# Optimization experiments

Measured on AMD Instinct MI355X. Metric: run time of the kernel, lower is better.

The kernel has to match this reference:

```python
import math
import jax, jax.numpy as jnp
import numpy as np

ALPHA = 1.000001   # sparsity_alpha
N_ITER = 50        # entmax_bisect default bisection iterations
EPS = 1e-40        # training-mode epsilon inside log

B, T = 2, 1024
V, C, H, L = 50304, 768, 12, 4
DINT = 64
INT_BIAS0 = 5.0


def _entmax_impl(X):
    # alpha-entmax over last dim via bisection (entmax package algorithm)
    am1 = ALPHA - 1.0
    d = X.shape[-1]
    Xs = X * am1
    max_val = jnp.max(Xs, axis=-1, keepdims=True)
    tau_lo = max_val - 1.0
    tau_hi = max_val - (1.0 / d) ** am1
    f_lo = jnp.sum(jnp.clip(Xs - tau_lo, 0.0) ** (1.0 / am1), axis=-1, keepdims=True) - 1.0
    dm = tau_hi - tau_lo
    p_m = jnp.zeros_like(Xs)
    for _ in range(N_ITER):
        dm = dm * 0.5
        tau_m = tau_lo + dm
        p_m = jnp.clip(Xs - tau_m, 0.0) ** (1.0 / am1)
        f_m = jnp.sum(p_m, axis=-1, keepdims=True) - 1.0
        tau_lo = jnp.where(f_m * f_lo >= 0, tau_m, tau_lo)
    return p_m / jnp.sum(p_m, axis=-1, keepdims=True)


@jax.custom_vjp
def entmax_bisect(X):
    return _entmax_impl(X)


def _entmax_fwd(X):
    Y = _entmax_impl(X)
    return Y, Y


def _entmax_bwd(Y, dY):
    # exact entmax jacobian-vector product (as in the torch entmax package)
    gppr = jnp.where(Y > 0, Y ** (2.0 - ALPHA), 0.0)
    dX = dY * gppr
    q = jnp.sum(dX, axis=-1, keepdims=True) / jnp.sum(gppr, axis=-1, keepdims=True)
    return (dX - q * gppr,)


entmax_bisect.defvjp(_entmax_fwd, _entmax_bwd)


def layer_norm(x, w, b):
    mu = jnp.mean(x, axis=-1, keepdims=True)
    var = jnp.mean((x - mu) ** 2, axis=-1, keepdims=True)
    return (x - mu) / jnp.sqrt(var + 1e-5) * w + b


def new_gelu(x):
    return 0.5 * x * (1.0 + jnp.tanh(math.sqrt(2.0 / math.pi) * (x + 0.044715 * x ** 3)))


def gpt_forward(wte, wpe, ln1_w, ln1_b, attn_w, attn_b, qint_w, kint_w, int_bias,
                proj_w, proj_b, ln2_w, ln2_b, fc_w, fc_b, fc2_w, fc2_b,
                lnf_w, lnf_b, idx):
    Bc, Tc = idx.shape
    hd = C // H
    x = wte[idx] + wpe[:Tc][None]                       # [B,T,C]
    i = jnp.arange(Tc)
    strict_lower = i[:, None] > i[None, :]              # bias_int = tril(diag=-1)
    causal = i[:, None] >= i[None, :]                   # bias = tril
    prev_mask = None
    for l in range(L):
        h = layer_norm(x, ln1_w[l], ln1_b[l])
        qkv = h @ attn_w[l].T + attn_b[l]
        q, k, v = jnp.split(qkv, 3, axis=-1)
        q = q.reshape(Bc, Tc, H, hd).transpose(0, 2, 1, 3)
        k = k.reshape(Bc, Tc, H, hd).transpose(0, 2, 1, 3)
        v = v.reshape(Bc, Tc, H, hd).transpose(0, 2, 1, 3)
        # integer-gate scores
        q_int = h @ qint_w[l].T                         # [B,T,DINT]
        k_int = h @ kint_w[l].T
        raw = jnp.einsum('bqd,bkd->bqk', q_int, k_int) / math.sqrt(DINT) + int_bias[l]
        raw2 = jnp.stack([raw, jnp.zeros_like(raw)], axis=-1)[:, None]  # [B,1,T,T,2]
        p_int = entmax_bisect(raw2.astype(jnp.float32))[..., 0]        # [B,1,T,T]
        p_int = jnp.where(strict_lower[None, None], p_int, 1.0)         # fill j>=i with 1
        cumprobs = jnp.cumprod(p_int, axis=-2)                          # cumprod over queries
        attn_mask = jnp.log(cumprobs + EPS)
        if prev_mask is not None:                        # propagate_in_depth=True
            attn_mask = attn_mask + prev_mask
        attn_mask = jnp.where(causal[None, None], attn_mask, -jnp.inf)
        scores = jnp.einsum('bhqd,bhkd->bhqk', q, k) / math.sqrt(hd) + attn_mask
        att = jax.nn.softmax(scores, axis=-1)
        y = jnp.einsum('bhqk,bhkd->bhqd', att, v)
        y = y.transpose(0, 2, 1, 3).reshape(Bc, Tc, C)
        y = y @ proj_w[l].T + proj_b[l]
        x = x + y
        h2 = layer_norm(x, ln2_w[l], ln2_b[l])
        x = x + (new_gelu(h2 @ fc_w[l].T + fc_b[l]) @ fc2_w[l].T + fc2_b[l])
        prev_mask = attn_mask
    x = layer_norm(x, lnf_w, lnf_b)
    return x @ wte.T                                     # weight-tied lm_head


def setup_inputs() -> dict:
    key = jax.random.key(0)
    ks = jax.random.split(key, 9)
    f32 = jnp.float32
    return {
        'wte': jax.random.normal(ks[0], (V, C), f32) * 0.02,
        'wpe': jax.random.normal(ks[1], (1024, C), f32) * 0.02,
        'ln1_w': jnp.ones((L, C), f32),
        'ln1_b': jnp.zeros((L, C), f32),
        'attn_w': jax.random.normal(ks[2], (L, 3 * C, C), f32) * 0.02,
        'attn_b': jnp.zeros((L, 3 * C), f32),
        'qint_w': jax.random.normal(ks[3], (L, DINT, C), f32) / math.sqrt(C),
        'kint_w': jax.random.normal(ks[4], (L, DINT, C), f32) / math.sqrt(C),
        'int_bias': jnp.full((L,), INT_BIAS0, f32),
        'proj_w': jax.random.normal(ks[5], (L, C, C), f32) * (0.02 / math.sqrt(2 * L)),
        'proj_b': jnp.zeros((L, C), f32),
        'ln2_w': jnp.ones((L, C), f32),
        'ln2_b': jnp.zeros((L, C), f32),
        'fc_w': jax.random.normal(ks[6], (L, 4 * C, C), f32) * 0.02,
        'fc_b': jnp.zeros((L, 4 * C), f32),
        'fc2_w': jax.random.normal(ks[7], (L, C, 4 * C), f32) * (0.02 / math.sqrt(2 * L)),
        'fc2_b': jnp.zeros((L, C), f32),
        'lnf_w': jnp.ones((C,), f32),
        'lnf_b': jnp.zeros((C,), f32),
        'idx': jax.random.randint(ks[8], (B, T), 0, V, dtype=jnp.int32),
    }


def reference(wte, wpe, ln1_w, ln1_b, attn_w, attn_b, qint_w, kint_w, int_bias,
              proj_w, proj_b, ln2_w, ln2_b, fc_w, fc_b, fc2_w, fc2_b,
              lnf_w, lnf_b, idx):
    return gpt_forward(wte, wpe, ln1_w, ln1_b, attn_w, attn_b, qint_w, kint_w,
                       int_bias, proj_w, proj_b, ln2_w, ln2_b, fc_w, fc_b,
                       fc2_w, fc2_b, lnf_w, lnf_b, idx)
```

## Files before the change

### kernel.cpp

```cpp
#include <hip/hip_runtime.h>


using f32x4  = __attribute__((ext_vector_type(4))) float;
using bf16x8 = __attribute__((ext_vector_type(8))) __bf16;
typedef unsigned short u16;
typedef unsigned int   u32;

#define B_  2
#define T_  1024
#define C_  768
#define H_  12
#define HD_ 64
#define L_  4
#define V_  50304

__device__ __forceinline__ u16 f2bf(float f){
  u32 u = __float_as_uint(f);
  u += 0x7fffu + ((u >> 16) & 1u);
  return (u16)(u >> 16);
}

__device__ __forceinline__ void gld_lds16(const u16* gsrc, u16* ldsbase){
  __builtin_amdgcn_global_load_lds(
      (const __attribute__((address_space(1))) void*)gsrc,
      (__attribute__((address_space(3))) void*)ldsbase, 16, 0, 0);
}

__global__ __launch_bounds__(256) void f2bf_vec(const float4* __restrict__ src,
                                                ushort4* __restrict__ dst){
  long i = (long)blockIdx.x * 256 + threadIdx.x;
  float4 v = src[i];
  ushort4 o;
  o.x = f2bf(v.x); o.y = f2bf(v.y); o.z = f2bf(v.z); o.w = f2bf(v.w);
  dst[i] = o;
}

__global__ __launch_bounds__(256) void build_wint(const float* __restrict__ qint_w,
                                                  const float* __restrict__ kint_w,
                                                  u16* __restrict__ wint){
  long i = (long)blockIdx.x * 256 + threadIdx.x;
  int c  = (int)(i % 768);
  long r = i / 768;
  int rr = (int)(r & 127);
  int l  = (int)(r >> 7);
  const float* src = (rr < 64) ? qint_w : kint_w;
  wint[i] = f2bf(src[((long)l * 64 + (rr & 63)) * 768 + c]);
}

__global__ __launch_bounds__(256) void embed_kernel(const float* __restrict__ wte,
                                                    const float* __restrict__ wpe,
                                                    const int* __restrict__ idx,
                                                    float* __restrict__ x){
  int row = blockIdx.x;
  int t   = row & (T_ - 1);
  int id  = idx[row];
  const float* ws = wte + (long)id * C_;
  const float* ps = wpe + (long)t  * C_;
  float* xr = x + (long)row * C_;
  for (int c = threadIdx.x; c < C_; c += 256) xr[c] = ws[c] + ps[c];
}

__global__ __launch_bounds__(256) void layernorm_bf16(const float* __restrict__ x,
                                                      const float* __restrict__ w,
                                                      const float* __restrict__ bsh,
                                                      u16* __restrict__ out){
  int row = blockIdx.x;
  const float* xr = x + (long)row * C_;
  int tid = threadIdx.x;
  float v[3], s = 0.f, ss = 0.f;
  #pragma unroll
  for (int k = 0; k < 3; ++k){
    float t = xr[tid + k * 256];
    v[k] = t; s += t; ss += t * t;
  }
  #pragma unroll
  for (int off = 1; off < 64; off <<= 1){
    s  += __shfl_xor(s,  off, 64);
    ss += __shfl_xor(ss, off, 64);
  }
  __shared__ float red[8];
  int wid = tid >> 6, lane = tid & 63;
  if (lane == 0){ red[wid] = s; red[4 + wid] = ss; }
  __syncthreads();
  s  = red[0] + red[1] + red[2] + red[3];
  ss = red[4] + red[5] + red[6] + red[7];
  float mu   = s * (1.f / C_);
  float var  = ss * (1.f / C_) - mu * mu;
  float rstd = rsqrtf(var + 1e-5f);
  u16* outr = out + (long)row * C_;
  #pragma unroll
  for (int k = 0; k < 3; ++k){
    int c = tid + k * 256;
    outr[c] = f2bf((v[k] - mu) * rstd * w[c] + bsh[c]);
  }
}

template<int BM, int BN, int WM, int WN, bool GELU>
__global__ __launch_bounds__(256) void gemm_nt(
    const u16* __restrict__ A, const u16* __restrict__ B, float* __restrict__ C,
    const float* __restrict__ bias, const float* __restrict__ addsrc,
    int K, int lda, int ldb, int ldc,
    long batchA, long batchB, long batchC, float alpha)
{
  constexpr int BK = 32;
  __shared__ __align__(16) u16 As[BM * BK];
  __shared__ __align__(16) u16 Bs[BN * BK];
  const int z = blockIdx.z;
  A += (long)z * batchA;
  B += (long)z * batchB;
  float* Cz = C + (long)z * batchC;
  const float* addz = addsrc ? addsrc + (long)z * batchC : nullptr;

  const int gx = gridDim.x, gy = gridDim.y;
  const int nwg = gx * gy;
  int bid = blockIdx.y * gx + blockIdx.x;
  {
    int xcd = bid & 7, pos = bid >> 3;
    int q = nwg >> 3, r = nwg & 7;
    bid = (xcd < r ? xcd * (q + 1) : r * (q + 1) + (xcd - r) * q) + pos;
  }
  const int by = bid % gy;
  const int bx = bid / gy;
  const int n0 = bx * BN, m0 = by * BM;

  const int tid = threadIdx.x, lane = tid & 63, wid = tid >> 6;
  const int l15 = lane & 15, quad = lane >> 4;
  constexpr int WCOLS = BN / WN;
  const int wrow = wid / WCOLS, wcol = wid % WCOLS;
  constexpr int FM = WM / 16, FN = WN / 16;
  f32x4 acc[FM][FN] = {};
  const int ktiles = K / BK;

  constexpr int SEGA = BM / 16;
  constexpr int SEGB = BN / 16;
  const int srow = lane >> 2;
  const int scol = (lane & 3) * 8;

  for (int kt = 0; kt < ktiles; ++kt){
    #pragma unroll
    for (int s = wid; s < SEGA; s += 4)
      gld_lds16(A + (long)(m0 + s * 16 + srow) * lda + kt * BK + scol,
                &As[s * 512]);
    #pragma unroll
    for (int s = wid; s < SEGB; s += 4)
      gld_lds16(B + (long)(n0 + s * 16 + srow) * ldb + kt * BK + scol,
                &Bs[s * 512]);
    __syncthreads();
    bf16x8 af[FM], bfr[FN];
    #pragma unroll
    for (int fm = 0; fm < FM; ++fm)
      af[fm] = *(const bf16x8*)&As[(wrow * WM + fm * 16 + l15) * BK + quad * 8];
    #pragma unroll
    for (int fn = 0; fn < FN; ++fn)
      bfr[fn] = *(const bf16x8*)&Bs[(wcol * WN + fn * 16 + l15) * BK + quad * 8];
    #pragma unroll
    for (int fm = 0; fm < FM; ++fm)
      #pragma unroll
      for (int fn = 0; fn < FN; ++fn)
        acc[fm][fn] = __builtin_amdgcn_mfma_f32_16x16x32_bf16(af[fm], bfr[fn],
                                                              acc[fm][fn], 0, 0, 0);
    __syncthreads();
  }
  #pragma unroll
  for (int fm = 0; fm < FM; ++fm){
    const int rowb = m0 + wrow * WM + fm * 16 + quad * 4;
    #pragma unroll
    for (int fn = 0; fn < FN; ++fn){
      const int col = n0 + wcol * WN + fn * 16 + l15;
      const float bv = bias ? bias[col] : 0.f;
      #pragma unroll
      for (int r = 0; r < 4; ++r){
        float v = acc[fm][fn][r] * alpha + bv;
        if (GELU)
          v = 0.5f * v * (1.f + tanhf(0.7978845608028654f * (v + 0.044715f * v * v * v)));
        const long off = (long)(rowb + r) * ldc + col;
        if (addz) v += addz[off];
        Cz[off] = v;
      }
    }
  }
}

__global__ __launch_bounds__(256) void lp_cumsum(const float* __restrict__ raw,
                                                 const float* __restrict__ int_bias,
                                                 int layer, float* __restrict__ Macc){
  constexpr int CT  = 8;
  constexpr int RG  = 32;
  constexpr int RPT = T_ / RG;
  const int tid = threadIdx.x;
  const int c   = tid & (CT - 1);
  const int g   = tid >> 3;
  const int gc  = blockIdx.x * CT + c;
  const int b   = gc >> 10;
  const int k   = gc & (T_ - 1);
  const float bias = int_bias[layer];
  const float* rb = raw  + (long)b * T_ * T_;
  float*       Mb = Macc + (long)b * T_ * T_;
  const int q0 = g * RPT;

  float lp[RPT];
  float s = 0.f;
  #pragma unroll
  for (int i = 0; i < RPT; ++i){
    int q = q0 + i;
    float z = rb[(long)q * T_ + k] + bias;
    float v = 0.f;
    if (q > k) v = (z >= -30.f) ? -log1pf(__expf(-z)) : z;
    lp[i] = v;
    s += v;
  }
  __shared__ float sums[RG][CT];
  sums[g][c] = s;
  __syncthreads();
  float run = 0.f;
  for (int g2 = 0; g2 < g; ++g2) run += sums[g2][c];
  #pragma unroll
  for (int i = 0; i < RPT; ++i){
    int q = q0 + i;
    run += lp[i];
    long off = (long)q * T_ + k;
    if (layer == 0) Mb[off] = run;
    else            Mb[off] += run;
  }
}

__global__ __launch_bounds__(256) void reshape_qkv(const float* __restrict__ qkv,
                                                   u16* __restrict__ qb,
                                                   u16* __restrict__ kb,
                                                   u16* __restrict__ vT){
  int row = blockIdx.x;
  int b = row >> 10, t = row & (T_ - 1);
  const float* src = qkv + (long)row * 2304;
  for (int i = threadIdx.x; i < C_; i += 256){
    int h = i >> 6, d = i & 63;
    long bh = (long)b * H_ + h;
    qb[(bh * T_ + t) * HD_ + d] = f2bf(src[i]);
    kb[(bh * T_ + t) * HD_ + d] = f2bf(src[C_ + i]);
    vT[(bh * HD_ + d) * T_ + t] = f2bf(src[2 * C_ + i]);
  }
}

__global__ __launch_bounds__(256) void attn_kernel(const u16* __restrict__ qb,
                                                   const u16* __restrict__ kb,
                                                   const u16* __restrict__ vT,
                                                   const float* __restrict__ Macc,
                                                   u16* __restrict__ ybf){
  __shared__ __align__(16) u16 P[4][16 * 72];
  const int qt = blockIdx.x, bh = blockIdx.y;
  const int b = bh / H_, h = bh % H_;
  const int tid = threadIdx.x, wid = tid >> 6, lane = tid & 63;
  const int l15 = lane & 15, quad = lane >> 4;
  const int qbase = qt * 64 + wid * 16;

  const u16* qrow = qb + ((long)bh * T_ + qbase + l15) * HD_;
  bf16x8 aq0 = *(const bf16x8*)(qrow + quad * 8);
  bf16x8 aq1 = *(const bf16x8*)(qrow + 32 + quad * 8);

  float mrow[4], lrow[4];
  f32x4 oacc[4] = {};
  #pragma unroll
  for (int r = 0; r < 4; ++r){ mrow[r] = -1e30f; lrow[r] = 0.f; }

  const float* Mb = Macc + (long)b * T_ * T_;
  const int ntiles = qt + 1;
  for (int kt = 0; kt < ntiles; ++kt){
    f32x4 s[4];
    #pragma unroll
    for (int fn = 0; fn < 4; ++fn){
      const u16* krow = kb + ((long)bh * T_ + kt * 64 + fn * 16 + l15) * HD_;
      bf16x8 bk0 = *(const bf16x8*)(krow + quad * 8);
      bf16x8 bk1 = *(const bf16x8*)(krow + 32 + quad * 8);
      f32x4 t = {};
      t = __builtin_amdgcn_mfma_f32_16x16x32_bf16(aq0, bk0, t, 0, 0, 0);
      t = __builtin_amdgcn_mfma_f32_16x16x32_bf16(aq1, bk1, t, 0, 0, 0);
      s[fn] = t;
    }
    float pv[4][4], tmax[4];
    #pragma unroll
    for (int r = 0; r < 4; ++r) tmax[r] = -1e30f;
    #pragma unroll
    for (int fn = 0; fn < 4; ++fn){
      int col = kt * 64 + fn * 16 + l15;
      #pragma unroll
      for (int r = 0; r < 4; ++r){
        int row = qbase + quad * 4 + r;
        float v = (col <= row) ? s[fn][r] * 0.125f + Mb[(long)row * T_ + col]
                               : -1e30f;
        pv[fn][r] = v;
        tmax[r] = fmaxf(tmax[r], v);
      }
    }
    #pragma unroll
    for (int r = 0; r < 4; ++r){
      float v = tmax[r];
      v = fmaxf(v, __shfl_xor(v, 1, 16));
      v = fmaxf(v, __shfl_xor(v, 2, 16));
      v = fmaxf(v, __shfl_xor(v, 4, 16));
      v = fmaxf(v, __shfl_xor(v, 8, 16));
      tmax[r] = v;
    }
    float alp[4], rsum[4];
    #pragma unroll
    for (int r = 0; r < 4; ++r){
      float mnew = fmaxf(mrow[r], tmax[r]);
      alp[r] = __expf(mrow[r] - mnew);
      mrow[r] = mnew;
      rsum[r] = 0.f;
    }
    #pragma unroll
    for (int fn = 0; fn < 4; ++fn)
      #pragma unroll
      for (int r = 0; r < 4; ++r){
        float p = __expf(pv[fn][r] - mrow[r]);
        pv[fn][r] = p;
        rsum[r] += p;
      }
    #pragma unroll
    for (int r = 0; r < 4; ++r){
      float v = rsum[r];
      v += __shfl_xor(v, 1, 16);
      v += __shfl_xor(v, 2, 16);
      v += __shfl_xor(v, 4, 16);
      v += __shfl_xor(v, 8, 16);
      lrow[r] = lrow[r] * alp[r] + v;
    }
    #pragma unroll
    for (int fn = 0; fn < 4; ++fn)
      #pragma unroll
      for (int r = 0; r < 4; ++r)
        P[wid][(quad * 4 + r) * 72 + fn * 16 + l15] = f2bf(pv[fn][r]);
    #pragma unroll
    for (int fn = 0; fn < 4; ++fn)
      #pragma unroll
      for (int r = 0; r < 4; ++r)
        oacc[fn][r] *= alp[r];
    bf16x8 ap0 = *(const bf16x8*)&P[wid][l15 * 72 + quad * 8];
    bf16x8 ap1 = *(const bf16x8*)&P[wid][l15 * 72 + 32 + quad * 8];
    #pragma unroll
    for (int fn = 0; fn < 4; ++fn){
      const u16* vrow = vT + ((long)bh * HD_ + fn * 16 + l15) * T_ + kt * 64;
      bf16x8 bv0 = *(const bf16x8*)(vrow + quad * 8);
      bf16x8 bv1 = *(const bf16x8*)(vrow + 32 + quad * 8);
      oacc[fn] = __builtin_amdgcn_mfma_f32_16x16x32_bf16(ap0, bv0, oacc[fn], 0, 0, 0);
      oacc[fn] = __builtin_amdgcn_mfma_f32_16x16x32_bf16(ap1, bv1, oacc[fn], 0, 0, 0);
    }
  }
  #pragma unroll
  for (int fn = 0; fn < 4; ++fn)
    #pragma unroll
    for (int r = 0; r < 4; ++r){
      int row = qbase + quad * 4 + r;
      int d   = fn * 16 + l15;
      float o = oacc[fn][r] / lrow[r];
      ybf[((long)b * T_ + row) * C_ + h * HD_ + d] = f2bf(o);
    }
}

extern "C" void kernel_launch(void* const* d_in, const int* in_sizes, int n_in,
                              void* d_out, int out_size, void* d_ws, size_t ws_size,
                              hipStream_t stream)
{
  (void)in_sizes; (void)n_in; (void)out_size; (void)ws_size;
  const float* wte     = (const float*)d_in[0];
  const float* wpe     = (const float*)d_in[1];
  const float* ln1_w   = (const float*)d_in[2];
  const float* ln1_b   = (const float*)d_in[3];
  const float* attn_w  = (const float*)d_in[4];
  const float* attn_b  = (const float*)d_in[5];
  const float* qint_w  = (const float*)d_in[6];
  const float* kint_w  = (const float*)d_in[7];
  const float* int_bias= (const float*)d_in[8];
  const float* proj_w  = (const float*)d_in[9];
  const float* proj_b  = (const float*)d_in[10];
  const float* ln2_w   = (const float*)d_in[11];
  const float* ln2_b   = (const float*)d_in[12];
  const float* fc_w    = (const float*)d_in[13];
  const float* fc_b    = (const float*)d_in[14];
  const float* fc2_w   = (const float*)d_in[15];
  const float* fc2_b   = (const float*)d_in[16];
  const float* lnf_w   = (const float*)d_in[17];
  const float* lnf_b   = (const float*)d_in[18];
  const int*   idx     = (const int*)d_in[19];
  float* out = (float*)d_out;

  char* p = (char*)d_ws;
  auto alloc = [&](long bytes) -> char* {
    char* r = p; p += (bytes + 255) & ~255L; return r;
  };
  u16*   wte_bf   = (u16*)  alloc((long)V_ * C_ * 2);
  u16*   attnw_bf = (u16*)  alloc((long)L_ * 3 * C_ * C_ * 2);
  u16*   wint_bf  = (u16*)  alloc((long)L_ * 128 * C_ * 2);
  u16*   projw_bf = (u16*)  alloc((long)L_ * C_ * C_ * 2);
  u16*   fcw_bf   = (u16*)  alloc((long)L_ * 4 * C_ * C_ * 2);
  u16*   fc2w_bf  = (u16*)  alloc((long)L_ * C_ * 4 * C_ * 2);
  float* x        = (float*)alloc((long)B_ * T_ * C_ * 4);
  u16*   hbf      = (u16*)  alloc((long)B_ * T_ * C_ * 2);
  float* qkv      = (float*)alloc((long)B_ * T_ * 3 * C_ * 4);
  float* qkint    = (float*)alloc((long)B_ * T_ * 128 * 4);
  u16*   qkintbf  = (u16*)  alloc((long)B_ * T_ * 128 * 2);
  float* raw      = (float*)alloc((long)B_ * T_ * T_ * 4);
  float* Macc     = (float*)alloc((long)B_ * T_ * T_ * 4);
  u16*   qb       = (u16*)  alloc((long)B_ * H_ * T_ * HD_ * 2);
  u16*   kb       = (u16*)  alloc((long)B_ * H_ * T_ * HD_ * 2);
  u16*   vT       = (u16*)  alloc((long)B_ * H_ * T_ * HD_ * 2);
  u16*   ybf      = (u16*)  alloc((long)B_ * T_ * C_ * 2);
  float* ff       = (float*)alloc((long)B_ * T_ * 4 * C_ * 4);
  u16*   ffbf     = (u16*)  alloc((long)B_ * T_ * 4 * C_ * 2);

  auto conv = [&](const float* s, u16* d, long n){
    f2bf_vec<<<(int)(n / 1024), 256, 0, stream>>>((const float4*)s, (ushort4*)d);
  };
  conv(wte,    wte_bf,   (long)V_ * C_);
  conv(attn_w, attnw_bf, (long)L_ * 3 * C_ * C_);
  conv(proj_w, projw_bf, (long)L_ * C_ * C_);
  conv(fc_w,   fcw_bf,   (long)L_ * 4 * C_ * C_);
  conv(fc2_w,  fc2w_bf,  (long)L_ * C_ * 4 * C_);
  build_wint<<<(L_ * 128 * C_) / 256, 256, 0, stream>>>(qint_w, kint_w, wint_bf);

  embed_kernel<<<B_ * T_, 256, 0, stream>>>(wte, wpe, idx, x);

  const int M = B_ * T_;
  for (int l = 0; l < L_; ++l){
    layernorm_bf16<<<M, 256, 0, stream>>>(x, ln1_w + l * C_, ln1_b + l * C_, hbf);
    gemm_nt<128,128,64,64,false><<<dim3(2304/128, M/128), 256, 0, stream>>>(
        hbf, attnw_bf + (long)l * 3 * C_ * C_, qkv, attn_b + l * 3 * C_, nullptr,
        C_, C_, C_, 3 * C_, 0, 0, 0, 1.f);
    gemm_nt<64,64,32,32,false><<<dim3(128/64, M/64), 256, 0, stream>>>(
        hbf, wint_bf + (long)l * 128 * C_, qkint, nullptr, nullptr,
        C_, C_, C_, 128, 0, 0, 0, 1.f);
    conv(qkint, qkintbf, (long)M * 128);
    gemm_nt<128,128,64,64,false><<<dim3(T_/128, T_/128, B_), 256, 0, stream>>>(
        qkintbf, qkintbf + 64, raw, nullptr, nullptr,
        64, 128, 128, T_, (long)T_ * 128, (long)T_ * 128, (long)T_ * T_, 0.125f);
    lp_cumsum<<<(B_ * T_) / 8, 256, 0, stream>>>(raw, int_bias, l, Macc);
    reshape_qkv<<<M, 256, 0, stream>>>(qkv, qb, kb, vT);
    attn_kernel<<<dim3(T_/64, B_ * H_), 256, 0, stream>>>(qb, kb, vT, Macc, ybf);
    gemm_nt<128,128,64,64,false><<<dim3(C_/128, M/128), 256, 0, stream>>>(
        ybf, projw_bf + (long)l * C_ * C_, x, proj_b + l * C_, x,
        C_, C_, C_, C_, 0, 0, 0, 1.f);
    layernorm_bf16<<<M, 256, 0, stream>>>(x, ln2_w + l * C_, ln2_b + l * C_, hbf);
    gemm_nt<128,128,64,64,true><<<dim3(4*C_/128, M/128), 256, 0, stream>>>(
        hbf, fcw_bf + (long)l * 4 * C_ * C_, ff, fc_b + l * 4 * C_, nullptr,
        C_, C_, C_, 4 * C_, 0, 0, 0, 1.f);
    conv(ff, ffbf, (long)M * 4 * C_);
    gemm_nt<128,128,64,64,false><<<dim3(C_/128, M/128), 256, 0, stream>>>(
        ffbf, fc2w_bf + (long)l * C_ * 4 * C_, x, fc2_b + l * C_, x,
        4 * C_, 4 * C_, 4 * C_, C_, 0, 0, 0, 1.f);
  }
  layernorm_bf16<<<M, 256, 0, stream>>>(x, lnf_w, lnf_b, hbf);
  gemm_nt<128,128,64,64,false><<<dim3(V_/128, M/128), 256, 0, stream>>>(
      hbf, wte_bf, out, nullptr, nullptr,
      C_, C_, C_, V_, 0, 0, 0, 1.f);
}
```

Baseline: 2.297 ms.

## Double-buffer GEMM LDS loads, emit bf16 outputs directly, tile-transpose V

The GEMM kernel now uses two LDS buffers. It prefetches the next K tile with global_load_lds while computing the current one, using explicit vmcnt waits and raw barriers. A new OMODE template selects bf16 output in the GEMM epilogue, so the QKV, qk-int and FC GEMMs write bf16 directly and the separate f32-to-bf16 conversion passes and f32 buffers are removed. The V transpose moves into its own LDS-tiled kernel for coalesced writes. The costs are doubled LDS per block, which may lower occupancy, and reliance on hand-counted vmcnt values.

```diff
diff --git a/kernel.cpp b/kernel.cpp
--- a/kernel.cpp
+++ b/kernel.cpp
@@ -95,21 +95,20 @@
   }
 }
 
-template<int BM, int BN, int WM, int WN, bool GELU>
+template<int BM, int BN, int WM, int WN, bool GELU, int OMODE>
 __global__ __launch_bounds__(256) void gemm_nt(
-    const u16* __restrict__ A, const u16* __restrict__ B, float* __restrict__ C,
+    const u16* __restrict__ A, const u16* __restrict__ B, void* __restrict__ Cv,
     const float* __restrict__ bias, const float* __restrict__ addsrc,
     int K, int lda, int ldb, int ldc,
     long batchA, long batchB, long batchC, float alpha)
 {
   constexpr int BK = 32;
-  __shared__ __align__(16) u16 As[BM * BK];
-  __shared__ __align__(16) u16 Bs[BN * BK];
+  constexpr int TILEA = BM * BK, TILEB = BN * BK;
+  __shared__ __align__(16) u16 As[2 * TILEA];
+  __shared__ __align__(16) u16 Bs[2 * TILEB];
   const int z = blockIdx.z;
   A += (long)z * batchA;
   B += (long)z * batchB;
-  float* Cz = C + (long)z * batchC;
-  const float* addz = addsrc ? addsrc + (long)z * batchC : nullptr;
 
   const int gx = gridDim.x, gy = gridDim.y;
   const int nwg = gx * gy;
@@ -133,34 +132,52 @@
 
   constexpr int SEGA = BM / 16;
   constexpr int SEGB = BN / 16;
+  constexpr int NLD = SEGA / 4 + SEGB / 4;
   const int srow = lane >> 2;
   const int scol = (lane & 3) * 8;
 
-  for (int kt = 0; kt < ktiles; ++kt){
+  auto stage = [&](int kt, int buf){
     #pragma unroll
     for (int s = wid; s < SEGA; s += 4)
       gld_lds16(A + (long)(m0 + s * 16 + srow) * lda + kt * BK + scol,
-                &As[s * 512]);
+                &As[buf * TILEA + s * 512]);
     #pragma unroll
     for (int s = wid; s < SEGB; s += 4)
       gld_lds16(B + (long)(n0 + s * 16 + srow) * ldb + kt * BK + scol,
-                &Bs[s * 512]);
-    __syncthreads();
+                &Bs[buf * TILEB + s * 512]);
+  };
+
+  stage(0, 0);
+  for (int kt = 0; kt < ktiles; ++kt){
+    const int cur = kt & 1;
+    if (kt + 1 < ktiles){
+      stage(kt + 1, cur ^ 1);
+      asm volatile("s_waitcnt vmcnt(%0)" :: "i"(NLD) : "memory");
+    } else {
+      asm volatile("s_waitcnt vmcnt(0)" ::: "memory");
+    }
+    __builtin_amdgcn_s_barrier();
+    __builtin_amdgcn_sched_barrier(0);
     bf16x8 af[FM], bfr[FN];
     #pragma unroll
     for (int fm = 0; fm < FM; ++fm)
-      af[fm] = *(const bf16x8*)&As[(wrow * WM + fm * 16 + l15) * BK + quad * 8];
+      af[fm] = *(const bf16x8*)&As[cur * TILEA +
+                                   (wrow * WM + fm * 16 + l15) * BK + quad * 8];
     #pragma unroll
     for (int fn = 0; fn < FN; ++fn)
-      bfr[fn] = *(const bf16x8*)&Bs[(wcol * WN + fn * 16 + l15) * BK + quad * 8];
+      bfr[fn] = *(const bf16x8*)&Bs[cur * TILEB +
+                                    (wcol * WN + fn * 16 + l15) * BK + quad * 8];
     #pragma unroll
     for (int fm = 0; fm < FM; ++fm)
       #pragma unroll
       for (int fn = 0; fn < FN; ++fn)
         acc[fm][fn] = __builtin_amdgcn_mfma_f32_16x16x32_bf16(af[fm], bfr[fn],
                                                               acc[fm][fn], 0, 0, 0);
-    __syncthreads();
-  }
+    __builtin_amdgcn_sched_barrier(0);
+    __builtin_amdgcn_s_barrier();
+    __builtin_amdgcn_sched_barrier(0);
+  }
+
   #pragma unroll
   for (int fm = 0; fm < FM; ++fm){
     const int rowb = m0 + wrow * WM + fm * 16 + quad * 4;
@@ -174,8 +191,14 @@
         if (GELU)
           v = 0.5f * v * (1.f + tanhf(0.7978845608028654f * (v + 0.044715f * v * v * v)));
         const long off = (long)(rowb + r) * ldc + col;
-        if (addz) v += addz[off];
-        Cz[off] = v;
+        if (OMODE == 0){
+          float* Cz = (float*)Cv + (long)z * batchC;
+          if (addsrc) v += addsrc[(long)z * batchC + off];
+          Cz[off] = v;
+        } else {
+          u16* Cz = (u16*)Cv + (long)z * batchC;
+          Cz[off] = f2bf(v);
+        }
       }
     }
   }
@@ -224,19 +247,44 @@
   }
 }
 
-__global__ __launch_bounds__(256) void reshape_qkv(const float* __restrict__ qkv,
-                                                   u16* __restrict__ qb,
-                                                   u16* __restrict__ kb,
-                                                   u16* __restrict__ vT){
+__global__ __launch_bounds__(256) void reshape_qk(const u16* __restrict__ qkv,
+                                                  u16* __restrict__ qb,
+                                                  u16* __restrict__ kb){
   int row = blockIdx.x;
   int b = row >> 10, t = row & (T_ - 1);
-  const float* src = qkv + (long)row * 2304;
+  const u16* src = qkv + (long)row * 2304;
   for (int i = threadIdx.x; i < C_; i += 256){
     int h = i >> 6, d = i & 63;
     long bh = (long)b * H_ + h;
-    qb[(bh * T_ + t) * HD_ + d] = f2bf(src[i]);
-    kb[(bh * T_ + t) * HD_ + d] = f2bf(src[C_ + i]);
-    vT[(bh * HD_ + d) * T_ + t] = f2bf(src[2 * C_ + i]);
+    qb[(bh * T_ + t) * HD_ + d] = src[i];
+    kb[(bh * T_ + t) * HD_ + d] = src[C_ + i];
+  }
+}
+
+__global__ __launch_bounds__(256) void transpose_v(const u16* __restrict__ qkv,
+                                                   u16* __restrict__ vT){
+  __shared__ u16 tile[64][65];
+  const int bh = blockIdx.x;
+  const int b = bh / H_, h = bh % H_;
+  const int t0 = blockIdx.y * 64;
+  const int tid = threadIdx.x;
+  const int tl = tid >> 6;
+  const int dl = tid & 63;
+  #pragma unroll
+  for (int i = 0; i < 16; ++i){
+    int t = t0 + tl * 16 + i;
+    tile[dl][tl * 16 + i] = qkv[(long)(b * T_ + t) * 2304 + 2 * C_ + h * 64 + dl];
+  }
+  __syncthreads();
+  const int dr = tid >> 2;
+  const int tc = (tid & 3) * 16;
+  u16* dst = vT + ((long)bh * HD_ + dr) * T_ + t0 + tc;
+  #pragma unroll
+  for (int c = 0; c < 16; c += 4){
+    ushort4 o;
+    o.x = tile[dr][tc + c];     o.y = tile[dr][tc + c + 1];
+    o.z = tile[dr][tc + c + 2]; o.w = tile[dr][tc + c + 3];
+    *(ushort4*)(dst + c) = o;
   }
 }
 
@@ -395,8 +443,7 @@
   u16*   fc2w_bf  = (u16*)  alloc((long)L_ * C_ * 4 * C_ * 2);
   float* x        = (float*)alloc((long)B_ * T_ * C_ * 4);
   u16*   hbf      = (u16*)  alloc((long)B_ * T_ * C_ * 2);
-  float* qkv      = (float*)alloc((long)B_ * T_ * 3 * C_ * 4);
-  float* qkint    = (float*)alloc((long)B_ * T_ * 128 * 4);
+  u16*   qkv      = (u16*)  alloc((long)B_ * T_ * 3 * C_ * 2);
   u16*   qkintbf  = (u16*)  alloc((long)B_ * T_ * 128 * 2);
   float* raw      = (float*)alloc((long)B_ * T_ * T_ * 4);
   float* Macc     = (float*)alloc((long)B_ * T_ * T_ * 4);
@@ -404,7 +451,6 @@
   u16*   kb       = (u16*)  alloc((long)B_ * H_ * T_ * HD_ * 2);
   u16*   vT       = (u16*)  alloc((long)B_ * H_ * T_ * HD_ * 2);
   u16*   ybf      = (u16*)  alloc((long)B_ * T_ * C_ * 2);
-  float* ff       = (float*)alloc((long)B_ * T_ * 4 * C_ * 4);
   u16*   ffbf     = (u16*)  alloc((long)B_ * T_ * 4 * C_ * 2);
 
   auto conv = [&](const float* s, u16* d, long n){
@@ -422,33 +468,32 @@
   const int M = B_ * T_;
   for (int l = 0; l < L_; ++l){
     layernorm_bf16<<<M, 256, 0, stream>>>(x, ln1_w + l * C_, ln1_b + l * C_, hbf);
-    gemm_nt<128,128,64,64,false><<<dim3(2304/128, M/128), 256, 0, stream>>>(
+    gemm_nt<128,128,64,64,false,1><<<dim3(2304/128, M/128), 256, 0, stream>>>(
         hbf, attnw_bf + (long)l * 3 * C_ * C_, qkv, attn_b + l * 3 * C_, nullptr,
         C_, C_, C_, 3 * C_, 0, 0, 0, 1.f);
-    gemm_nt<64,64,32,32,false><<<dim3(128/64, M/64), 256, 0, stream>>>(
-        hbf, wint_bf + (long)l * 128 * C_, qkint, nullptr, nullptr,
+    gemm_nt<64,64,32,32,false,1><<<dim3(128/64, M/64), 256, 0, stream>>>(
+        hbf, wint_bf + (long)l * 128 * C_, qkintbf, nullptr, nullptr,
         C_, C_, C_, 128, 0, 0, 0, 1.f);
-    conv(qkint, qkintbf, (long)M * 128);
-    gemm_nt<128,128,64,64,false><<<dim3(T_/128, T_/128, B_), 256, 0, stream>>>(
+    gemm_nt<128,128,64,64,false,0><<<dim3(T_/128, T_/128, B_), 256, 0, stream>>>(
         qkintbf, qkintbf + 64, raw, nullptr, nullptr,
         64, 128, 128, T_, (long)T_ * 128, (long)T_ * 128, (long)T_ * T_, 0.125f);
     lp_cumsum<<<(B_ * T_) / 8, 256, 0, stream>>>(raw, int_bias, l, Macc);
-    reshape_qkv<<<M, 256, 0, stream>>>(qkv, qb, kb, vT);
+    reshape_qk<<<M, 256, 0, stream>>>(qkv, qb, kb);
+    transpose_v<<<dim3(B_ * H_, T_ / 64), 256, 0, stream>>>(qkv, vT);
     attn_kernel<<<dim3(T_/64, B_ * H_), 256, 0, stream>>>(qb, kb, vT, Macc, ybf);
-    gemm_nt<128,128,64,64,false><<<dim3(C_/128, M/128), 256, 0, stream>>>(
+    gemm_nt<128,128,64,64,false,0><<<dim3(C_/128, M/128), 256, 0, stream>>>(
         ybf, projw_bf + (long)l * C_ * C_, x, proj_b + l * C_, x,
         C_, C_, C_, C_, 0, 0, 0, 1.f);
     layernorm_bf16<<<M, 256, 0, stream>>>(x, ln2_w + l * C_, ln2_b + l * C_, hbf);
-    gemm_nt<128,128,64,64,true><<<dim3(4*C_/128, M/128), 256, 0, stream>>>(
-        hbf, fcw_bf + (long)l * 4 * C_ * C_, ff, fc_b + l * 4 * C_, nullptr,
+    gemm_nt<128,128,64,64,true,1><<<dim3(4*C_/128, M/128), 256, 0, stream>>>(
+        hbf, fcw_bf + (long)l * 4 * C_ * C_, ffbf, fc_b + l * 4 * C_, nullptr,
         C_, C_, C_, 4 * C_, 0, 0, 0, 1.f);
-    conv(ff, ffbf, (long)M * 4 * C_);
-    gemm_nt<128,128,64,64,false><<<dim3(C_/128, M/128), 256, 0, stream>>>(
+    gemm_nt<128,128,64,64,false,0><<<dim3(C_/128, M/128), 256, 0, stream>>>(
         ffbf, fc2w_bf + (long)l * C_ * 4 * C_, x, fc2_b + l * C_, x,
         4 * C_, 4 * C_, 4 * C_, C_, 0, 0, 0, 1.f);
   }
   layernorm_bf16<<<M, 256, 0, stream>>>(x, lnf_w, lnf_b, hbf);
-  gemm_nt<128,128,64,64,false><<<dim3(V_/128, M/128), 256, 0, stream>>>(
+  gemm_nt<128,128,64,64,false,0><<<dim3(V_/128, M/128), 256, 0, stream>>>(
       hbf, wte_bf, out, nullptr, nullptr,
       C_, C_, C_, V_, 0, 0, 0, 1.f);
 }
```

After: 1.986 ms. 13.5% less time.
